# Kernel tuning notes

Measured on AMD Instinct MI355X. Metric: run time of the kernel, lower is better.

## Reference

```python
import jax, jax.numpy as jnp
import numpy as np

HEADS = 8
DIM_HEAD = 64
H = W = 32  # height = width = int(sqrt(num_patches)) = 32; n = 1024 tokens
N = H * W
TABLE = (2 * H - 1) * (2 * W - 1)  # 3969
NEG_THRESH = 0.9
GATE = -2.0  # non-trainable gate parameter


def _build_rel_index_dis():
    # valid 2D relative-position index in [0, TABLE) and normalized squared distance
    coords = np.stack(np.meshgrid(np.arange(H), np.arange(W), indexing='ij'))  # (2,H,W)
    flat = coords.reshape(2, -1)  # (2, N)
    rel = flat[:, :, None] - flat[:, None, :]  # (2, N, N)
    dis = (rel[0] / H) ** 2 + (rel[1] / W) ** 2
    idx = (rel[0] + H - 1) * (2 * W - 1) + (rel[1] + W - 1)
    return idx.astype(np.int32), dis.astype(np.float32)


def setup_inputs() -> dict:
    key = jax.random.key(0)
    ks = jax.random.split(key, 8)
    b, n, dim = 4, N, 512
    inner = HEADS * DIM_HEAD
    rel_index, dis = _build_rel_index_dis()
    return {
        'x': jax.random.normal(ks[0], (b, n, dim), jnp.float32),
        'prob': jax.random.uniform(ks[1], (b, n), jnp.float32),
        'W_qkv': jax.random.normal(ks[2], (dim, 3 * inner), jnp.float32) * 0.02,
        'table1': jax.random.normal(ks[3], (TABLE, HEADS), jnp.float32) * 0.02,
        'table2': jax.random.normal(ks[4], (TABLE, HEADS), jnp.float32) * 0.02,
        'headsita': jnp.arange(1, HEADS + 1, dtype=jnp.float32) * 0.1,
        'W_thresh': jax.random.normal(ks[5], (DIM_HEAD, 1), jnp.float32) * 0.02,
        'W_out': jax.random.normal(ks[6], (inner, 512), jnp.float32) * 0.02,
        'b_out': jnp.zeros((512,), jnp.float32),
        'rel_index': jnp.asarray(rel_index),
        'dis': jnp.asarray(dis),
    }


def reference(x, prob, W_qkv, table1, table2, headsita, W_thresh, W_out, b_out, rel_index, dis):
    b, n, dim = x.shape
    scale = DIM_HEAD ** -0.5
    qkv = x @ W_qkv  # (b, n, 3*inner)
    q, k, v = jnp.split(qkv, 3, axis=-1)
    split_heads = lambda t: t.reshape(b, n, HEADS, DIM_HEAD).transpose(0, 2, 1, 3)
    q, k, v = split_heads(q), split_heads(k), split_heads(v)  # (b, h, n, d)

    dots0 = jnp.einsum('bhid,bhjd->bhij', q, k) * scale  # (b, h, n, n)

    # dual RPE bias: product of two table gathers with shared index -> (h, n, n)
    bias = (table1[rel_index] * table2[rel_index]).transpose(2, 0, 1)
    factor = 1.0 / (2.0 * headsita ** 2 + 1e-6)  # (h,)
    pos_embed = jnp.exp(-factor[:, None, None] * dis[None, :, :])  # (h, n, n)
    dots = dots0 + bias[None] + 0.01 * pos_embed[None]

    attn = jax.nn.softmax(dots, axis=-1)
    attn_max = jnp.max(attn, axis=-1)  # (b, h, n)
    attn_min = jnp.min(attn, axis=-1)

    # per-query dynamic threshold, gated
    thresh_raw = jax.nn.sigmoid(jnp.einsum('bhnd,do->bhn', q, W_thresh)) * jax.nn.sigmoid(GATE)
    thresh = attn_min + thresh_raw * (attn_max - attn_min)  # (b, h, n)

    record = (attn - thresh[..., None] > 0).astype(attn.dtype)  # (b, h, n, n)
    # zero out query rows where prob >= NEG_THRESH
    record = jnp.where(prob[:, None, :, None] >= NEG_THRESH, 0.0, record)

    deno = jnp.einsum('bhij,bhij->bhi', attn, record)
    attn_pruned = attn * record / (deno[..., None] + 1e-6)

    out = jnp.einsum('bhij,bhjd->bhid', attn_pruned, v)  # (b, h, n, d)
    out = out.transpose(0, 2, 1, 3).reshape(b, n, HEADS * DIM_HEAD)
    out = out @ W_out + b_out
    attn0 = jax.nn.softmax(dots0, axis=-1)
    return out, attn0
```

## Files before the change

kernel.cpp:

```cpp
#include <hip/hip_runtime.h>
#include <cmath>

#define NTOK 1024
#define NH 8
#define DH 64
#define BATCH 4
#define TBL 3969

#define L2E 1.4426950408889634f

typedef __attribute__((ext_vector_type(8))) short short8;
typedef __attribute__((ext_vector_type(4))) float f32x4;

__device__ __forceinline__ unsigned bf16rne(float x) {
  unsigned u = __float_as_uint(x);
  return (u + 0x7fffu + ((u >> 16) & 1u)) >> 16;
}

__device__ __forceinline__ void cvt2(float a, float b, unsigned& h, unsigned& l) {
  asm("v_cvt_pk_bf16_f32 %0, %1, %2" : "=v"(h) : "v"(a), "v"(b));
  float ra = a - __uint_as_float(h << 16);
  float rb = b - __uint_as_float(h & 0xffff0000u);
  asm("v_cvt_pk_bf16_f32 %0, %1, %2" : "=v"(l) : "v"(ra), "v"(rb));
}

__device__ __forceinline__ void split8_pk(const float* v, short8& h8, short8& l8) {
  union { short8 s; unsigned u[4]; } H, L;
#pragma unroll
  for (int j = 0; j < 4; ++j) {
    unsigned hp, lp;
    cvt2(v[2 * j], v[2 * j + 1], hp, lp);
    H.u[j] = hp; L.u[j] = lp;
  }
  h8 = H.s; l8 = L.s;
}

__device__ __forceinline__ f32x4 mfma16(short8 a, short8 b, f32x4 c) {
  return __builtin_amdgcn_mfma_f32_16x16x32_bf16(a, b, c, 0, 0, 0);
}

__device__ __forceinline__ void gload16(const unsigned short* g, unsigned short* l) {
  __builtin_amdgcn_global_load_lds(
      (__attribute__((address_space(1))) unsigned int*)(g),
      (__attribute__((address_space(3))) unsigned int*)(l), 16, 0, 0);
}

__global__ void k_comb(const float* __restrict__ t1, const float* __restrict__ t2,
                       const float* __restrict__ sita, const float* __restrict__ dis,
                       float* __restrict__ comb, float* __restrict__ combe) {
  int idx = blockIdx.x * 256 + threadIdx.x;
  if (idx >= TBL) return;
  int dy = idx / 63 - 31, dx = idx % 63 - 31;
  int yi = dy > 0 ? dy : 0, yj = dy > 0 ? 0 : -dy;
  int xi = dx > 0 ? dx : 0, xj = dx > 0 ? 0 : -dx;
  float dv = dis[(size_t)(yi * 32 + xi) * NTOK + (yj * 32 + xj)];
#pragma unroll
  for (int h = 0; h < NH; ++h) {
    float ita = sita[h];
    float factor = 1.0f / (2.0f * ita * ita + 1e-6f);
    float bi = t1[idx * 8 + h] * t2[idx * 8 + h];
    float v = bi + 0.01f * expf(-factor * dv);
    comb[(size_t)h * TBL + idx] = v * L2E;
    combe[(size_t)h * TBL + idx] = expf(v);
  }
}

__global__ __launch_bounds__(256) void k_prep(
    const float* __restrict__ x, const float* __restrict__ wqkv,
    const float* __restrict__ wout,
    unsigned short* __restrict__ xh, unsigned short* __restrict__ xl,
    unsigned short* __restrict__ wth, unsigned short* __restrict__ wtl,
    unsigned short* __restrict__ wouth, unsigned short* __restrict__ woutl) {
  const int bid = blockIdx.x;
  const int t = threadIdx.x;
  if (bid < 1024) {
    size_t base = ((size_t)bid * 256 + t) * 8;
    float v8[8];
    *(float4*)(v8) = *(const float4*)(x + base);
    *(float4*)(v8 + 4) = *(const float4*)(x + base + 4);
    short8 h8, l8;
    split8_pk(v8, h8, l8);
    *(short8*)(xh + base) = h8;
    *(short8*)(xl + base) = l8;
    return;
  }
  __shared__ float tile[64][65];
  const float* src;
  unsigned short *dh, *dl;
  int n0, k0, N;
  if (bid < 1216) {
    int b2 = bid - 1024;
    n0 = (b2 % 24) * 64; k0 = (b2 / 24) * 64; N = 1536;
    src = wqkv; dh = wth; dl = wtl;
  } else {
    int b2 = bid - 1216;
    n0 = (b2 % 8) * 64; k0 = (b2 / 8) * 64; N = 512;
    src = wout; dh = wouth; dl = woutl;
  }
#pragma unroll
  for (int l = 0; l < 4; ++l) {
    int idx = t + l * 256;
    int r = idx >> 4, c4 = idx & 15;
    float4 v = *(const float4*)(src + (size_t)(k0 + r) * N + n0 + c4 * 4);
    tile[r][c4 * 4 + 0] = v.x; tile[r][c4 * 4 + 1] = v.y;
    tile[r][c4 * 4 + 2] = v.z; tile[r][c4 * 4 + 3] = v.w;
  }
  __syncthreads();
#pragma unroll
  for (int l = 0; l < 2; ++l) {
    int idx = t + l * 256;
    int n = idx >> 3, c8 = idx & 7;
    float v8[8];
#pragma unroll
    for (int j = 0; j < 8; ++j) v8[j] = tile[c8 * 8 + j][n];
    short8 h8, l8;
    split8_pk(v8, h8, l8);
    *(short8*)(dh + (size_t)(n0 + n) * 512 + k0 + c8 * 8) = h8;
    *(short8*)(dl + (size_t)(n0 + n) * 512 + k0 + c8 * 8) = l8;
  }
}

__device__ __forceinline__ void gemm_core(
    const unsigned short* pAh, const unsigned short* pAl,
    const unsigned short* pBh, const unsigned short* pBl,
    int a0, int b0, int w, int lane, f32x4 acc[4][4],
    unsigned short* AhS, unsigned short* AlS,
    unsigned short* BhS, unsigned short* BlS) {
  const int q = lane >> 4, li = lane & 15;
  const int wr = w >> 1, wc = w & 1;
#pragma unroll 1
  for (int k0 = 0; k0 < 512; k0 += 64) {
#pragma unroll
    for (int l = 0; l < 4; ++l) {
      int idx = w * 256 + l * 64 + lane;
      int row = idx >> 3, u = idx & 7;
      int so = k0 + ((u ^ (row & 7)) * 8);
      int db = (w * 256 + l * 64) * 8;
      gload16(pAh + (size_t)(a0 + row) * 512 + so, AhS + db);
      gload16(pAl + (size_t)(a0 + row) * 512 + so, AlS + db);
      gload16(pBh + (size_t)(b0 + row) * 512 + so, BhS + db);
      gload16(pBl + (size_t)(b0 + row) * 512 + so, BlS + db);
    }
    __syncthreads();
#pragma unroll
    for (int c = 0; c < 2; ++c) {
      short8 aH[4], aL[4], bH[4], bL[4];
#pragma unroll
      for (int mt = 0; mt < 4; ++mt) {
        int row = 64 * wr + 16 * mt + li;
        int ro = row * 64 + (((4 * c + q) ^ (row & 7)) * 8);
        aH[mt] = *(const short8*)(AhS + ro);
        aL[mt] = *(const short8*)(AlS + ro);
        int rowb = 64 * wc + 16 * mt + li;
        int rob = rowb * 64 + (((4 * c + q) ^ (rowb & 7)) * 8);
        bH[mt] = *(const short8*)(BhS + rob);
        bL[mt] = *(const short8*)(BlS + rob);
      }
#pragma unroll
      for (int mt = 0; mt < 4; ++mt)
#pragma unroll
        for (int nt = 0; nt < 4; ++nt) {
          acc[mt][nt] = mfma16(aH[mt], bH[nt], acc[mt][nt]);
          acc[mt][nt] = mfma16(aH[mt], bL[nt], acc[mt][nt]);
          acc[mt][nt] = mfma16(aL[mt], bH[nt], acc[mt][nt]);
        }
    }
    __syncthreads();
  }
}

__global__ __launch_bounds__(256, 2) void k_qkv(
    const unsigned short* __restrict__ xh, const unsigned short* __restrict__ xl,
    const unsigned short* __restrict__ wth, const unsigned short* __restrict__ wtl,
    float* __restrict__ qf, unsigned short* __restrict__ kspl,
    unsigned short* __restrict__ vspl) {
  __shared__ unsigned short AhS[8192], AlS[8192], BhS[8192], BlS[8192];
  const int bx = blockIdx.x, by = blockIdx.y;
  const int part = bx >> 2;
  const int t = threadIdx.x;
  const int w = t >> 6, lane = t & 63;
  const int q = lane >> 4, li = lane & 15;
  const int wr = w >> 1, wc = w & 1;
  f32x4 acc[4][4] = {};
  if (part < 2)
    gemm_core(wth, wtl, xh, xl, bx * 128, by * 128, w, lane, acc, AhS, AlS, BhS, BlS);
  else
    gemm_core(xh, xl, wth, wtl, by * 128, bx * 128, w, lane, acc, AhS, AlS, BhS, BlS);

  if (part == 0) {
    int hq = bx * 2 + wr;
#pragma unroll
    for (int nt = 0; nt < 4; ++nt) {
      int tok = by * 128 + 64 * wc + 16 * nt + li;
      int b = tok >> 10, i = tok & 1023;
#pragma unroll
      for (int mt = 0; mt < 4; ++mt) {
        int d0 = 16 * mt + 4 * q;
        float4 v;
        v.x = acc[mt][nt][0]; v.y = acc[mt][nt][1];
        v.z = acc[mt][nt][2]; v.w = acc[mt][nt][3];
        *(float4*)(qf + ((size_t)(b * NH + hq) * NTOK + i) * DH + d0) = v;
      }
    }
  } else if (part == 1) {
    int hq = bx * 2 + wr - 8;
#pragma unroll
    for (int nt = 0; nt < 4; ++nt) {
      int tok = by * 128 + 64 * wc + 16 * nt + li;
      int b = tok >> 10, tile = (tok & 1023) >> 6, tl = tok & 63;
      unsigned short* kb = kspl + ((size_t)((b * NH + hq) * 16 + tile) * 2) * 4096;
#pragma unroll
      for (int mt = 0; mt < 4; ++mt) {
        int d0 = 16 * mt + 4 * q;
        int pu = (d0 >> 3) ^ (tl & 7), off = d0 & 7;
        unsigned h0, h1, l0, l1;
        cvt2(acc[mt][nt][0], acc[mt][nt][1], h0, l0);
        cvt2(acc[mt][nt][2], acc[mt][nt][3], h1, l1);
        *(uint2*)(kb + tl * 64 + pu * 8 + off) = make_uint2(h0, h1);
        *(uint2*)(kb + 4096 + tl * 64 + pu * 8 + off) = make_uint2(l0, l1);
      }
    }
  } else {
    int hq = (bx - 8) * 2 + wc;
#pragma unroll
    for (int mt = 0; mt < 4; ++mt) {
      int tok0 = by * 128 + 64 * wr + 16 * mt + 4 * q;
      int b = tok0 >> 10, tile = (tok0 & 1023) >> 6, tl0 = tok0 & 63;
      int lu = tl0 >> 3, off = tl0 & 7;
#pragma unroll
      for (int nt = 0; nt < 4; ++nt) {
        int d = 16 * nt + li;
        unsigned short* vb = vspl + ((size_t)((b * NH + hq) * 16 + tile) * 2) * 4096;
        int pu = lu ^ (d & 7);
        unsigned h0, h1, l0, l1;
        cvt2(acc[mt][nt][0], acc[mt][nt][1], h0, l0);
        cvt2(acc[mt][nt][2], acc[mt][nt][3], h1, l1);
        *(uint2*)(vb + d * 64 + pu * 8 + off) = make_uint2(h0, h1);
        *(uint2*)(vb + 4096 + d * 64 + pu * 8 + off) = make_uint2(l0, l1);
      }
    }
  }
}

__global__ __launch_bounds__(256, 2) void k_attn(
    const float* __restrict__ qf, const unsigned short* __restrict__ kspl,
    const unsigned short* __restrict__ vspl, const float* __restrict__ prob,
    const float* __restrict__ comb, const float* __restrict__ combe,
    const float* __restrict__ wt,
    float* __restrict__ attn0, unsigned short* __restrict__ oh,
    unsigned short* __restrict__ ol) {
  __shared__ unsigned short KhS[4096], KlS[4096];
  __shared__ unsigned short VhS[4096], VlS[4096];
  __shared__ float PfS[64 * 68];
  __shared__ float2 csS[3 * 64];
  __shared__ float thrS[64];

  const int rt = blockIdx.x;
  const int bh = blockIdx.y;
  const int b = bh >> 3, h = bh & 7;
  const int i0 = rt * 64;
  const int t = threadIdx.x;
  const int w = t >> 6;
  const int lane = t & 63;
  const int q = lane >> 4, li = lane & 15;
  const float* qb = qf + (size_t)bh * NTOK * DH;
  const float* ch = comb + (size_t)h * TBL;
  const float* che = combe + (size_t)h * TBL;
  const int rbase = (i0 >> 5) + 30;

  {
    int row = t >> 2, dg = t & 3;
    const float* qr2 = qb + (size_t)(i0 + row) * DH + dg * 16;
    float sum = 0.f;
#pragma unroll
    for (int c = 0; c < 16; ++c) sum += qr2[c] * wt[dg * 16 + c];
    sum += __shfl_xor(sum, 1);
    sum += __shfl_xor(sum, 2);
    if (dg == 0)
      thrS[row] = (1.0f / (1.0f + exp2f(-sum * L2E))) * 0.11920292202211755f;
  }

  short8 qah[2], qal[2];
  {
    const float* qr2 = qb + (size_t)(i0 + 16 * w + li) * DH;
    const float QS = 0.125f * L2E;
#pragma unroll
    for (int c = 0; c < 2; ++c) {
      float4 a = *(const float4*)(qr2 + 32 * c + 8 * q);
      float4 bb = *(const float4*)(qr2 + 32 * c + 8 * q + 4);
      float tmp[8] = {a.x * QS, a.y * QS, a.z * QS, a.w * QS,
                      bb.x * QS, bb.y * QS, bb.z * QS, bb.w * QS};
      split8_pk(tmp, qah[c], qal[c]);
    }
  }

  float m0l[4], s0l[4], ml[4], sl[4], mnl[4];
#pragma unroll
  for (int r = 0; r < 4; ++r) {
    m0l[r] = -1e30f; ml[r] = -1e30f; mnl[r] = 1e30f;
    s0l[r] = 0.f; sl[r] = 0.f;
  }

#pragma unroll 1
  for (int j0 = 0; j0 < NTOK; j0 += 64) {
    const unsigned short* gk = kspl + ((size_t)(bh * 16 + (j0 >> 6)) * 2) * 4096;
#pragma unroll
    for (int jl = 0; jl < 2; ++jl) {
      int seg = 2 * w + jl;
      gload16(gk + seg * 512 + lane * 8, KhS + seg * 512);
      gload16(gk + 4096 + seg * 512 + lane * 8, KlS + seg * 512);
    }
    if (t < 192) {
      int rl2 = t >> 6, c2 = t & 63;
      if (c2 < 63) {
        int off = (rbase - (j0 >> 5) + rl2) * 63 + c2;
        csS[rl2 * 64 + c2] = make_float2(ch[off], che[off]);
      }
    }
    __syncthreads();

    f32x4 acc[4] = {};
#pragma unroll
    for (int c = 0; c < 2; ++c) {
#pragma unroll
      for (int T = 0; T < 4; ++T) {
        int ro = (16 * T + li) * 64 + ((4 * c + q) ^ (li & 7)) * 8;
        short8 bh8 = *(const short8*)(KhS + ro);
        short8 bl8 = *(const short8*)(KlS + ro);
        acc[T] = mfma16(qah[c], bh8, acc[T]);
        acc[T] = mfma16(qah[c], bl8, acc[T]);
        acc[T] = mfma16(qal[c], bh8, acc[T]);
      }
    }

    float2 ce[4][4];
    float t0[4], tt[4], tmn[4];
#pragma unroll
    for (int r = 0; r < 4; ++r) { t0[r] = -1e30f; tt[r] = -1e30f; tmn[r] = 1e30f; }
#pragma unroll
    for (int T = 0; T < 4; ++T) {
      int jj = 16 * T + li;
#pragma unroll
      for (int r = 0; r < 4; ++r) {
        int il = 16 * w + 4 * q + r;
        int rl2 = (il >> 5) - (jj >> 5) + 1;
        int cc2 = (il & 31) - (jj & 31) + 31;
        ce[T][r] = csS[rl2 * 64 + cc2];
        float d0 = acc[T][r];
        float dt = d0 + ce[T][r].x;
        t0[r] = fmaxf(t0[r], d0);
        tt[r] = fmaxf(tt[r], dt);
        tmn[r] = fminf(tmn[r], dt);
      }
    }
#pragma unroll
    for (int r = 0; r < 4; ++r) {
      float nm0 = fmaxf(m0l[r], t0[r]);
      float nm = fmaxf(ml[r], tt[r]);
      float sc0 = exp2f(m0l[r] - nm0), sc = exp2f(ml[r] - nm), k0 = exp2f(nm0 - nm);
      float s0a = 0.f, sEa = 0.f;
#pragma unroll
      for (int T = 0; T < 4; ++T) {
        float e0 = exp2f(acc[T][r] - nm0);
        s0a += e0;
        sEa += e0 * ce[T][r].y;
      }
      s0l[r] = s0l[r] * sc0 + s0a;
      sl[r] = sl[r] * sc + sEa * k0;
      m0l[r] = nm0; ml[r] = nm; mnl[r] = fminf(mnl[r], tmn[r]);
    }
    __syncthreads();
  }

  float m0f[4], is0f[4], thf[4], crf[4];
#pragma unroll
  for (int r = 0; r < 4; ++r) {
    float m0v = m0l[r], s0 = s0l[r], m = ml[r], s = sl[r], mn = mnl[r];
#pragma unroll
    for (int off = 1; off < 16; off <<= 1) {
      float om = __shfl_xor(m0v, off), os = __shfl_xor(s0, off);
      float n0 = fmaxf(m0v, om);
      s0 = s0 * exp2f(m0v - n0) + os * exp2f(om - n0);
      m0v = n0;
      float om2 = __shfl_xor(m, off), os2 = __shfl_xor(s, off);
      float n2 = fmaxf(m, om2);
      s = s * exp2f(m - n2) + os2 * exp2f(om2 - n2);
      m = n2;
      mn = fminf(mn, __shfl_xor(mn, off));
    }
    float isf = 1.f / s;
    float amin = exp2f(mn - m) * isf;
    int rloc = 16 * w + 4 * q + r;
    float th = amin + thrS[rloc] * (isf - amin);
    if (prob[b * NTOK + i0 + rloc] >= 0.9f) th = 1e30f;
    m0f[r] = m0v; is0f[r] = 1.f / s0; thf[r] = th; crf[r] = exp2f(m0v - m) * isf;
  }

  f32x4 oacc[4] = {};
  float denl[4] = {0.f, 0.f, 0.f, 0.f};
#pragma unroll 1
  for (int j0 = 0; j0 < NTOK; j0 += 64) {
    const unsigned short* gk = kspl + ((size_t)(bh * 16 + (j0 >> 6)) * 2) * 4096;
    const unsigned short* gv = vspl + ((size_t)(bh * 16 + (j0 >> 6)) * 2) * 4096;
#pragma unroll
    for (int jl = 0; jl < 2; ++jl) {
      int seg = 2 * w + jl;
      gload16(gk + seg * 512 + lane * 8, KhS + seg * 512);
      gload16(gk + 4096 + seg * 512 + lane * 8, KlS + seg * 512);
      gload16(gv + seg * 512 + lane * 8, VhS + seg * 512);
      gload16(gv + 4096 + seg * 512 + lane * 8, VlS + seg * 512);
    }
    if (t < 192) {
      int rl2 = t >> 6, c2 = t & 63;
      if (c2 < 63) {
        int off = (rbase - (j0 >> 5) + rl2) * 63 + c2;
        csS[rl2 * 64 + c2] = make_float2(ch[off], che[off]);
      }
    }
    __syncthreads();

    f32x4 acc[4] = {};
#pragma unroll
    for (int c = 0; c < 2; ++c) {
#pragma unroll
      for (int T = 0; T < 4; ++T) {
        int ro = (16 * T + li) * 64 + ((4 * c + q) ^ (li & 7)) * 8;
        short8 bh8 = *(const short8*)(KhS + ro);
        short8 bl8 = *(const short8*)(KlS + ro);
        acc[T] = mfma16(qah[c], bh8, acc[T]);
        acc[T] = mfma16(qah[c], bl8, acc[T]);
        acc[T] = mfma16(qal[c], bh8, acc[T]);
      }
    }

#pragma unroll
    for (int T = 0; T < 4; ++T) {
      int jj = 16 * T + li;
#pragma unroll
      for (int r = 0; r < 4; ++r) {
        int il = 16 * w + 4 * q + r;
        int rl2 = (il >> 5) - (jj >> 5) + 1;
        int cc2 = (il & 31) - (jj & 31) + 31;
        float ey = csS[rl2 * 64 + cc2].y;
        float e0 = exp2f(acc[T][r] - m0f[r]);
        __builtin_nontemporal_store(
            e0 * is0f[r],
            attn0 + (size_t)(bh * NTOK + i0 + il) * NTOK + j0 + jj);
        float at = e0 * ey * crf[r];
        float p = (at - thf[r] > 0.f) ? at : 0.f;
        denl[r] += p;
        PfS[il * 68 + jj] = p;
      }
    }
#pragma unroll
    for (int c = 0; c < 2; ++c) {
      const float* pp = PfS + (16 * w + li) * 68 + 32 * c + 8 * q;
      float pv8[8];
      *(float4*)(pv8) = *(const float4*)pp;
      *(float4*)(pv8 + 4) = *(const float4*)(pp + 4);
      short8 pah, pal;
      split8_pk(pv8, pah, pal);
#pragma unroll
      for (int T = 0; T < 4; ++T) {
        int ro = (16 * T + li) * 64 + ((4 * c + q) ^ (li & 7)) * 8;
        short8 vh8 = *(const short8*)(VhS + ro);
        short8 vl8 = *(const short8*)(VlS + ro);
        oacc[T] = mfma16(pah, vh8, oacc[T]);
        oacc[T] = mfma16(pah, vl8, oacc[T]);
        oacc[T] = mfma16(pal, vh8, oacc[T]);
      }
    }
    __syncthreads();
  }

#pragma unroll
  for (int r = 0; r < 4; ++r) {
    float dsum = denl[r];
#pragma unroll
    for (int off = 1; off < 16; off <<= 1) dsum += __shfl_xor(dsum, off);
    float pf = 1.f / (dsum + 1e-6f);
    int row = i0 + 16 * w + 4 * q + r;
    size_t rb2 = ((size_t)b * NTOK + row) * 512 + h * 64;
#pragma unroll
    for (int T = 0; T < 4; ++T) {
      float val = oacc[T][r] * pf;
      unsigned hv = bf16rne(val);
      float lo2 = val - __uint_as_float(hv << 16);
      oh[rb2 + 16 * T + li] = (unsigned short)hv;
      ol[rb2 + 16 * T + li] = (unsigned short)bf16rne(lo2);
    }
  }
}

__global__ __launch_bounds__(256, 2) void k_out(
    const unsigned short* __restrict__ wouth, const unsigned short* __restrict__ woutl,
    const unsigned short* __restrict__ oh, const unsigned short* __restrict__ ol,
    const float* __restrict__ bias, float* __restrict__ c) {
  __shared__ unsigned short AhS[8192], AlS[8192], BhS[8192], BlS[8192];
  const int bx = blockIdx.x, by = blockIdx.y;
  const int t = threadIdx.x;
  const int w = t >> 6, lane = t & 63;
  const int q = lane >> 4, li = lane & 15;
  const int wr = w >> 1, wc = w & 1;
  f32x4 acc[4][4] = {};
  gemm_core(wouth, woutl, oh, ol, bx * 128, by * 128, w, lane, acc, AhS, AlS, BhS, BlS);
#pragma unroll
  for (int mt = 0; mt < 4; ++mt) {
    int col0 = bx * 128 + 64 * wr + 16 * mt + 4 * q;
    float4 b4 = *(const float4*)(bias + col0);
#pragma unroll
    for (int nt = 0; nt < 4; ++nt) {
      int tok = by * 128 + 64 * wc + 16 * nt + li;
      float4 v;
      v.x = acc[mt][nt][0] + b4.x; v.y = acc[mt][nt][1] + b4.y;
      v.z = acc[mt][nt][2] + b4.z; v.w = acc[mt][nt][3] + b4.w;
      *(float4*)(c + (size_t)tok * 512 + col0) = v;
    }
  }
}

extern "C" void kernel_launch(void* const* d_in, const int* in_sizes, int n_in,
                              void* d_out, int out_size, void* d_ws, size_t ws_size,
                              hipStream_t stream) {
  const float* x    = (const float*)d_in[0];
  const float* prob = (const float*)d_in[1];
  const float* wqkv = (const float*)d_in[2];
  const float* t1   = (const float*)d_in[3];
  const float* t2   = (const float*)d_in[4];
  const float* sita = (const float*)d_in[5];
  const float* wt   = (const float*)d_in[6];
  const float* wout = (const float*)d_in[7];
  const float* bout = (const float*)d_in[8];
  const float* dis  = (const float*)d_in[10];

  float* out = (float*)d_out;
  float* attn0 = out + (size_t)BATCH * NTOK * 512;

  float* comb = (float*)d_ws;
  float* combe = comb + 32768;
  float* qf = combe + 32768;
  unsigned short* kspl = (unsigned short*)(qf + (size_t)BATCH * NH * NTOK * DH);
  unsigned short* vspl = kspl + (size_t)4194304;
  unsigned short* xh = vspl + (size_t)4194304;
  unsigned short* xl = xh + (size_t)2097152;
  unsigned short* wth = xl + (size_t)2097152;
  unsigned short* wtl = wth + (size_t)786432;
  unsigned short* wouth = wtl + (size_t)786432;
  unsigned short* woutl = wouth + (size_t)262144;
  unsigned short* oh = xh;
  unsigned short* ol = xl;

  hipLaunchKernelGGL(k_comb, dim3(16), dim3(256), 0, stream, t1, t2, sita, dis, comb, combe);
  hipLaunchKernelGGL(k_prep, dim3(1280), dim3(256), 0, stream,
                     x, wqkv, wout, xh, xl, wth, wtl, wouth, woutl);
  hipLaunchKernelGGL(k_qkv, dim3(12, 32), dim3(256), 0, stream,
                     xh, xl, wth, wtl, qf, kspl, vspl);
  hipLaunchKernelGGL(k_attn, dim3(16, 32), dim3(256), 0, stream,
                     qf, kspl, vspl, prob, comb, combe, wt, attn0, oh, ol);
  hipLaunchKernelGGL(k_out, dim3(4, 32), dim3(256), 0, stream,
                     wouth, woutl, oh, ol, bout, out);
}
```

Before: 281.4 us.

## Split attention key columns across wave pairs and remap block IDs across XCDs

The attention kernel moves to 512 threads, and each pair of waves splits the 64 key columns of a tile. Softmax statistics and the partial output and denominator are merged through shared memory. The aim is more waves in flight to hide latency and a shorter per-wave chain of MFMA and exp work. All three GEMM and attention kernels also switch to 1-D grids with an XCD-aware block-ID swizzle for better L2 locality. The cost is extra shared-memory reductions and barriers, plus register pressure under the tighter launch bounds.

```diff
diff --git a/kernel.cpp b/kernel.cpp
--- a/kernel.cpp
+++ b/kernel.cpp
@@ -175,7 +175,9 @@
     float* __restrict__ qf, unsigned short* __restrict__ kspl,
     unsigned short* __restrict__ vspl) {
   __shared__ unsigned short AhS[8192], AlS[8192], BhS[8192], BlS[8192];
-  const int bx = blockIdx.x, by = blockIdx.y;
+  const int bid = blockIdx.x;
+  const int lin = (bid & 7) * 48 + (bid >> 3);
+  const int by = lin / 12, bx = lin % 12;
   const int part = bx >> 2;
   const int t = threadIdx.x;
   const int w = t >> 6, lane = t & 63;
@@ -242,7 +244,7 @@
   }
 }
 
-__global__ __launch_bounds__(256, 2) void k_attn(
+__global__ __launch_bounds__(512, 4) void k_attn(
     const float* __restrict__ qf, const unsigned short* __restrict__ kspl,
     const unsigned short* __restrict__ vspl, const float* __restrict__ prob,
     const float* __restrict__ comb, const float* __restrict__ combe,
@@ -255,34 +257,39 @@
   __shared__ float2 csS[3 * 64];
   __shared__ float thrS[64];
 
-  const int rt = blockIdx.x;
-  const int bh = blockIdx.y;
+  const int bid = blockIdx.x;
+  const int lin = (bid & 7) * 64 + (bid >> 3);
+  const int bh = lin >> 4;
+  const int rt = lin & 15;
   const int b = bh >> 3, h = bh & 7;
   const int i0 = rt * 64;
   const int t = threadIdx.x;
   const int w = t >> 6;
   const int lane = t & 63;
   const int q = lane >> 4, li = lane & 15;
+  const int g = w >> 1;
+  const int cw = w & 1;
   const float* qb = qf + (size_t)bh * NTOK * DH;
   const float* ch = comb + (size_t)h * TBL;
   const float* che = combe + (size_t)h * TBL;
   const int rbase = (i0 >> 5) + 30;
 
   {
-    int row = t >> 2, dg = t & 3;
-    const float* qr2 = qb + (size_t)(i0 + row) * DH + dg * 16;
+    int row = t >> 3, dg = t & 7;
+    const float* qr2 = qb + (size_t)(i0 + row) * DH + dg * 8;
     float sum = 0.f;
 #pragma unroll
-    for (int c = 0; c < 16; ++c) sum += qr2[c] * wt[dg * 16 + c];
+    for (int c = 0; c < 8; ++c) sum += qr2[c] * wt[dg * 8 + c];
     sum += __shfl_xor(sum, 1);
     sum += __shfl_xor(sum, 2);
+    sum += __shfl_xor(sum, 4);
     if (dg == 0)
       thrS[row] = (1.0f / (1.0f + exp2f(-sum * L2E))) * 0.11920292202211755f;
   }
 
   short8 qah[2], qal[2];
   {
-    const float* qr2 = qb + (size_t)(i0 + 16 * w + li) * DH;
+    const float* qr2 = qb + (size_t)(i0 + 16 * g + li) * DH;
     const float QS = 0.125f * L2E;
 #pragma unroll
     for (int c = 0; c < 2; ++c) {
@@ -304,12 +311,8 @@
 #pragma unroll 1
   for (int j0 = 0; j0 < NTOK; j0 += 64) {
     const unsigned short* gk = kspl + ((size_t)(bh * 16 + (j0 >> 6)) * 2) * 4096;
-#pragma unroll
-    for (int jl = 0; jl < 2; ++jl) {
-      int seg = 2 * w + jl;
-      gload16(gk + seg * 512 + lane * 8, KhS + seg * 512);
-      gload16(gk + 4096 + seg * 512 + lane * 8, KlS + seg * 512);
-    }
+    gload16(gk + w * 512 + lane * 8, KhS + w * 512);
+    gload16(gk + 4096 + w * 512 + lane * 8, KlS + w * 512);
     if (t < 192) {
       int rl2 = t >> 6, c2 = t & 63;
       if (c2 < 63) {
@@ -319,35 +322,36 @@
     }
     __syncthreads();
 
-    f32x4 acc[4] = {};
+    f32x4 acc2[2] = {};
 #pragma unroll
     for (int c = 0; c < 2; ++c) {
 #pragma unroll
-      for (int T = 0; T < 4; ++T) {
+      for (int T2 = 0; T2 < 2; ++T2) {
+        int T = 2 * cw + T2;
         int ro = (16 * T + li) * 64 + ((4 * c + q) ^ (li & 7)) * 8;
         short8 bh8 = *(const short8*)(KhS + ro);
         short8 bl8 = *(const short8*)(KlS + ro);
-        acc[T] = mfma16(qah[c], bh8, acc[T]);
-        acc[T] = mfma16(qah[c], bl8, acc[T]);
-        acc[T] = mfma16(qal[c], bh8, acc[T]);
-      }
-    }
-
-    float2 ce[4][4];
+        acc2[T2] = mfma16(qah[c], bh8, acc2[T2]);
+        acc2[T2] = mfma16(qah[c], bl8, acc2[T2]);
+        acc2[T2] = mfma16(qal[c], bh8, acc2[T2]);
+      }
+    }
+
+    float2 ce[2][4];
     float t0[4], tt[4], tmn[4];
 #pragma unroll
     for (int r = 0; r < 4; ++r) { t0[r] = -1e30f; tt[r] = -1e30f; tmn[r] = 1e30f; }
 #pragma unroll
-    for (int T = 0; T < 4; ++T) {
-      int jj = 16 * T + li;
+    for (int T2 = 0; T2 < 2; ++T2) {
+      int jj = 16 * (2 * cw + T2) + li;
 #pragma unroll
       for (int r = 0; r < 4; ++r) {
-        int il = 16 * w + 4 * q + r;
+        int il = 16 * g + 4 * q + r;
         int rl2 = (il >> 5) - (jj >> 5) + 1;
         int cc2 = (il & 31) - (jj & 31) + 31;
-        ce[T][r] = csS[rl2 * 64 + cc2];
-        float d0 = acc[T][r];
-        float dt = d0 + ce[T][r].x;
+        ce[T2][r] = csS[rl2 * 64 + cc2];
+        float d0 = acc2[T2][r];
+        float dt = d0 + ce[T2][r].x;
         t0[r] = fmaxf(t0[r], d0);
         tt[r] = fmaxf(tt[r], dt);
         tmn[r] = fminf(tmn[r], dt);
@@ -360,10 +364,10 @@
       float sc0 = exp2f(m0l[r] - nm0), sc = exp2f(ml[r] - nm), k0 = exp2f(nm0 - nm);
       float s0a = 0.f, sEa = 0.f;
 #pragma unroll
-      for (int T = 0; T < 4; ++T) {
-        float e0 = exp2f(acc[T][r] - nm0);
+      for (int T2 = 0; T2 < 2; ++T2) {
+        float e0 = exp2f(acc2[T2][r] - nm0);
         s0a += e0;
-        sEa += e0 * ce[T][r].y;
+        sEa += e0 * ce[T2][r].y;
       }
       s0l[r] = s0l[r] * sc0 + s0a;
       sl[r] = sl[r] * sc + sEa * k0;
@@ -372,7 +376,7 @@
     __syncthreads();
   }
 
-  float m0f[4], is0f[4], thf[4], crf[4];
+  float M0[4], S0[4], M[4], S[4], MN[4];
 #pragma unroll
   for (int r = 0; r < 4; ++r) {
     float m0v = m0l[r], s0 = s0l[r], m = ml[r], s = sl[r], mn = mnl[r];
@@ -388,13 +392,36 @@
       m = n2;
       mn = fminf(mn, __shfl_xor(mn, off));
     }
+    M0[r] = m0v; S0[r] = s0; M[r] = m; S[r] = s; MN[r] = mn;
+  }
+  if (li == 0) {
+#pragma unroll
+    for (int r = 0; r < 4; ++r) {
+      int row = 16 * g + 4 * q + r;
+      float* p = PfS + (cw * 64 + row) * 5;
+      p[0] = M0[r]; p[1] = S0[r]; p[2] = M[r]; p[3] = S[r]; p[4] = MN[r];
+    }
+  }
+  __syncthreads();
+
+  float m0f[4], is0f[4], thf[4], crf[4];
+#pragma unroll
+  for (int r = 0; r < 4; ++r) {
+    int rloc = 16 * g + 4 * q + r;
+    const float* pa = PfS + rloc * 5;
+    const float* pb = PfS + (64 + rloc) * 5;
+    float m0v = fmaxf(pa[0], pb[0]);
+    float s0 = pa[1] * exp2f(pa[0] - m0v) + pb[1] * exp2f(pb[0] - m0v);
+    float m = fmaxf(pa[2], pb[2]);
+    float s = pa[3] * exp2f(pa[2] - m) + pb[3] * exp2f(pb[2] - m);
+    float mn = fminf(pa[4], pb[4]);
     float isf = 1.f / s;
     float amin = exp2f(mn - m) * isf;
-    int rloc = 16 * w + 4 * q + r;
     float th = amin + thrS[rloc] * (isf - amin);
     if (prob[b * NTOK + i0 + rloc] >= 0.9f) th = 1e30f;
     m0f[r] = m0v; is0f[r] = 1.f / s0; thf[r] = th; crf[r] = exp2f(m0v - m) * isf;
   }
+  __syncthreads();
 
   f32x4 oacc[4] = {};
   float denl[4] = {0.f, 0.f, 0.f, 0.f};
@@ -402,14 +429,10 @@
   for (int j0 = 0; j0 < NTOK; j0 += 64) {
     const unsigned short* gk = kspl + ((size_t)(bh * 16 + (j0 >> 6)) * 2) * 4096;
     const unsigned short* gv = vspl + ((size_t)(bh * 16 + (j0 >> 6)) * 2) * 4096;
-#pragma unroll
-    for (int jl = 0; jl < 2; ++jl) {
-      int seg = 2 * w + jl;
-      gload16(gk + seg * 512 + lane * 8, KhS + seg * 512);
-      gload16(gk + 4096 + seg * 512 + lane * 8, KlS + seg * 512);
-      gload16(gv + seg * 512 + lane * 8, VhS + seg * 512);
-      gload16(gv + 4096 + seg * 512 + lane * 8, VlS + seg * 512);
-    }
+    gload16(gk + w * 512 + lane * 8, KhS + w * 512);
+    gload16(gk + 4096 + w * 512 + lane * 8, KlS + w * 512);
+    gload16(gv + w * 512 + lane * 8, VhS + w * 512);
+    gload16(gv + 4096 + w * 512 + lane * 8, VlS + w * 512);
     if (t < 192) {
       int rl2 = t >> 6, c2 = t & 63;
       if (c2 < 63) {
@@ -419,30 +442,31 @@
     }
     __syncthreads();
 
-    f32x4 acc[4] = {};
+    f32x4 acc2[2] = {};
 #pragma unroll
     for (int c = 0; c < 2; ++c) {
 #pragma unroll
-      for (int T = 0; T < 4; ++T) {
+      for (int T2 = 0; T2 < 2; ++T2) {
+        int T = 2 * cw + T2;
         int ro = (16 * T + li) * 64 + ((4 * c + q) ^ (li & 7)) * 8;
         short8 bh8 = *(const short8*)(KhS + ro);
         short8 bl8 = *(const short8*)(KlS + ro);
-        acc[T] = mfma16(qah[c], bh8, acc[T]);
-        acc[T] = mfma16(qah[c], bl8, acc[T]);
-        acc[T] = mfma16(qal[c], bh8, acc[T]);
-      }
-    }
-
-#pragma unroll
-    for (int T = 0; T < 4; ++T) {
-      int jj = 16 * T + li;
+        acc2[T2] = mfma16(qah[c], bh8, acc2[T2]);
+        acc2[T2] = mfma16(qah[c], bl8, acc2[T2]);
+        acc2[T2] = mfma16(qal[c], bh8, acc2[T2]);
+      }
+    }
+
+#pragma unroll
+    for (int T2 = 0; T2 < 2; ++T2) {
+      int jj = 16 * (2 * cw + T2) + li;
 #pragma unroll
       for (int r = 0; r < 4; ++r) {
-        int il = 16 * w + 4 * q + r;
+        int il = 16 * g + 4 * q + r;
         int rl2 = (il >> 5) - (jj >> 5) + 1;
         int cc2 = (il & 31) - (jj & 31) + 31;
         float ey = csS[rl2 * 64 + cc2].y;
-        float e0 = exp2f(acc[T][r] - m0f[r]);
+        float e0 = exp2f(acc2[T2][r] - m0f[r]);
         __builtin_nontemporal_store(
             e0 * is0f[r],
             attn0 + (size_t)(bh * NTOK + i0 + il) * NTOK + j0 + jj);
@@ -452,9 +476,8 @@
         PfS[il * 68 + jj] = p;
       }
     }
-#pragma unroll
-    for (int c = 0; c < 2; ++c) {
-      const float* pp = PfS + (16 * w + li) * 68 + 32 * c + 8 * q;
+    {
+      const float* pp = PfS + (16 * g + li) * 68 + 32 * cw + 8 * q;
       float pv8[8];
       *(float4*)(pv8) = *(const float4*)pp;
       *(float4*)(pv8 + 4) = *(const float4*)(pp + 4);
@@ -462,7 +485,7 @@
       split8_pk(pv8, pah, pal);
 #pragma unroll
       for (int T = 0; T < 4; ++T) {
-        int ro = (16 * T + li) * 64 + ((4 * c + q) ^ (li & 7)) * 8;
+        int ro = (16 * T + li) * 64 + ((4 * cw + q) ^ (li & 7)) * 8;
         short8 vh8 = *(const short8*)(VhS + ro);
         short8 vl8 = *(const short8*)(VlS + ro);
         oacc[T] = mfma16(pah, vh8, oacc[T]);
@@ -475,19 +498,35 @@
 
 #pragma unroll
   for (int r = 0; r < 4; ++r) {
-    float dsum = denl[r];
-#pragma unroll
-    for (int off = 1; off < 16; off <<= 1) dsum += __shfl_xor(dsum, off);
-    float pf = 1.f / (dsum + 1e-6f);
-    int row = i0 + 16 * w + 4 * q + r;
-    size_t rb2 = ((size_t)b * NTOK + row) * 512 + h * 64;
-#pragma unroll
-    for (int T = 0; T < 4; ++T) {
-      float val = oacc[T][r] * pf;
-      unsigned hv = bf16rne(val);
-      float lo2 = val - __uint_as_float(hv << 16);
-      oh[rb2 + 16 * T + li] = (unsigned short)hv;
-      ol[rb2 + 16 * T + li] = (unsigned short)bf16rne(lo2);
+#pragma unroll
+    for (int off = 1; off < 16; off <<= 1) denl[r] += __shfl_xor(denl[r], off);
+  }
+  if (cw == 1) {
+#pragma unroll
+    for (int r = 0; r < 4; ++r) {
+      int row = 16 * g + 4 * q + r;
+#pragma unroll
+      for (int T = 0; T < 4; ++T) PfS[row * 68 + 16 * T + li] = oacc[T][r];
+      if (li == 0) PfS[row * 68 + 64] = denl[r];
+    }
+  }
+  __syncthreads();
+  if (cw == 0) {
+#pragma unroll
+    for (int r = 0; r < 4; ++r) {
+      int rloc = 16 * g + 4 * q + r;
+      float dsum = denl[r] + PfS[rloc * 68 + 64];
+      float pf = 1.f / (dsum + 1e-6f);
+      int row = i0 + rloc;
+      size_t rb2 = ((size_t)b * NTOK + row) * 512 + h * 64;
+#pragma unroll
+      for (int T = 0; T < 4; ++T) {
+        float val = (oacc[T][r] + PfS[rloc * 68 + 16 * T + li]) * pf;
+        unsigned hv = bf16rne(val);
+        float lo2 = val - __uint_as_float(hv << 16);
+        oh[rb2 + 16 * T + li] = (unsigned short)hv;
+        ol[rb2 + 16 * T + li] = (unsigned short)bf16rne(lo2);
+      }
     }
   }
 }
@@ -497,7 +536,9 @@
     const unsigned short* __restrict__ oh, const unsigned short* __restrict__ ol,
     const float* __restrict__ bias, float* __restrict__ c) {
   __shared__ unsigned short AhS[8192], AlS[8192], BhS[8192], BlS[8192];
-  const int bx = blockIdx.x, by = blockIdx.y;
+  const int bid = blockIdx.x;
+  const int lin = (bid & 7) * 16 + (bid >> 3);
+  const int by = lin >> 2, bx = lin & 3;
   const int t = threadIdx.x;
   const int w = t >> 6, lane = t & 63;
   const int q = lane >> 4, li = lane & 15;
@@ -553,10 +594,10 @@
   hipLaunchKernelGGL(k_comb, dim3(16), dim3(256), 0, stream, t1, t2, sita, dis, comb, combe);
   hipLaunchKernelGGL(k_prep, dim3(1280), dim3(256), 0, stream,
                      x, wqkv, wout, xh, xl, wth, wtl, wouth, woutl);
-  hipLaunchKernelGGL(k_qkv, dim3(12, 32), dim3(256), 0, stream,
+  hipLaunchKernelGGL(k_qkv, dim3(384), dim3(256), 0, stream,
                      xh, xl, wth, wtl, qf, kspl, vspl);
-  hipLaunchKernelGGL(k_attn, dim3(16, 32), dim3(256), 0, stream,
+  hipLaunchKernelGGL(k_attn, dim3(512), dim3(512), 0, stream,
                      qf, kspl, vspl, prob, comb, combe, wt, attn0, oh, ol);
-  hipLaunchKernelGGL(k_out, dim3(4, 32), dim3(256), 0, stream,
+  hipLaunchKernelGGL(k_out, dim3(128), dim3(256), 0, stream,
                      wouth, woutl, oh, ol, bout, out);
 }
```

Result: no change. 280.5 us (-0.3%).
